# Performance work log

Measured on AMD Instinct MI355X. Metric: run time of the kernel, lower is better.

Reference implementation:

```python
import jax, jax.numpy as jnp
import numpy as np

K = 24  # number of clusters (all ids in [0,K) assumed present per image)
DELTA_VAR = 1.0
DELTA_DIST = 2.0
VAR_W = 1.0
DIST_W = 1.0
REG_W = 1.0


def setup_inputs() -> dict:
    key = jax.random.key(0)
    k1, k2 = jax.random.split(key)
    data = jax.random.normal(k1, (4, 16, 512, 1024), dtype=jnp.float32)
    labels = jax.random.randint(k2, (4, 512, 1024), 0, K, dtype=jnp.int32)
    return {"data": data, "labels": labels}


def reference(data, labels):
    B, D, H, Wd = data.shape
    N = H * Wd
    # [B, N, D] points, [B*N] global segment ids (batch-offset cluster ids)
    X = jnp.transpose(data.reshape(B, D, N), (0, 2, 1)).reshape(B * N, D)
    seg = (labels.reshape(B, N) + jnp.arange(B, dtype=labels.dtype)[:, None] * K).reshape(-1)

    # per-cluster sums and counts -> centers  [B*K, D]
    sums = jax.ops.segment_sum(X, seg, num_segments=B * K)
    counts = jax.ops.segment_sum(jnp.ones((B * N,), X.dtype), seg, num_segments=B * K)
    centers_flat = sums / counts[:, None]
    centers = centers_flat.reshape(B, K, D)
    counts_bk = counts.reshape(B, K)

    # variance term: per-point hinged distance to own cluster center
    c_per_point = centers_flat[seg]                      # [B*N, D]
    pt_dist = jnp.linalg.norm(X - c_per_point, axis=1)   # [B*N]
    hv = jnp.maximum(pt_dist - DELTA_VAR, 0.0) ** 2
    var_per_cluster = jax.ops.segment_sum(hv, seg, num_segments=B * K).reshape(B, K) / counts_bk
    var_sum = var_per_cluster.sum()

    # distance term: pairwise center distances (diagonal kept, as in original,
    # contributing a constant delta_dist**2 per cluster)
    diff = centers[:, :, None, :] - centers[:, None, :, :]     # [B, K, K, D]
    sq = jnp.sum(diff * diff, axis=-1)                         # [B, K, K]
    eye = jnp.eye(K, dtype=bool)[None]
    cdist = jnp.where(eye, 0.0, jnp.sqrt(jnp.where(eye, 1.0, sq)))
    hd = jnp.maximum(DELTA_DIST - cdist, 0.0) ** 2
    dist_sum = hd.sum() / (2.0 * K * (K - 1))

    # regularization: mean center norm per image, summed over batch
    reg_sum = jnp.linalg.norm(centers, axis=2).mean(axis=1).sum()

    loss = (VAR_W * var_sum + DIST_W * dist_sum + REG_W * reg_sum) / B
    return loss
```

## Files before the change

### kernel.cpp

```cpp
#include <hip/hip_runtime.h>
#include <math.h>

#define KC 24
constexpr int D = 16;
constexpr int B = 4;
constexpr int N = 512 * 1024;
constexpr float DELTA_VAR = 1.0f;
constexpr float DELTA_DIST = 2.0f;

constexpr int REP = 8;
constexpr int RS  = KC * 17;
constexpr int CS  = 33;
constexpr int PTS = 1024;
constexpr int BLOCKS = (B * N) / PTS;


__global__ __launch_bounds__(256) void k_sums(const float* __restrict__ data,
                                              const int* __restrict__ labels,
                                              float* __restrict__ g_sums,
                                              float* __restrict__ g_cnt) {
    __shared__ float s_sum[REP * RS];
    __shared__ float s_cnt[REP * CS];
    const int t = threadIdx.x;
    for (int i = t; i < REP * RS; i += 256) s_sum[i] = 0.f;
    for (int i = t; i < REP * CS; i += 256) s_cnt[i] = 0.f;
    __syncthreads();

    const int chunk = blockIdx.x * PTS;
    const int b     = chunk >> 19;
    const int n0    = (chunk & (N - 1)) + t * 4;

    const int4 lab = *(const int4*)(labels + chunk + t * 4);
    const int rbase = (t & 7) * RS;
    const int ax = rbase + lab.x * 17;
    const int ay = rbase + lab.y * 17;
    const int az = rbase + lab.z * 17;
    const int aw = rbase + lab.w * 17;

    const float* base = data + (size_t)(b * D) * N + n0;
    float4 cur = *(const float4*)(base);
#pragma unroll
    for (int d = 0; d < D; ++d) {
        float4 nxt;
        if (d < D - 1) nxt = *(const float4*)(base + (size_t)(d + 1) * N);
        atomicAdd(&s_sum[ax + d], cur.x);
        atomicAdd(&s_sum[ay + d], cur.y);
        atomicAdd(&s_sum[az + d], cur.z);
        atomicAdd(&s_sum[aw + d], cur.w);
        cur = nxt;
    }
    const int cbase = (t & 7) * CS;
    atomicAdd(&s_cnt[cbase + lab.x], 1.f);
    atomicAdd(&s_cnt[cbase + lab.y], 1.f);
    atomicAdd(&s_cnt[cbase + lab.z], 1.f);
    atomicAdd(&s_cnt[cbase + lab.w], 1.f);
    __syncthreads();

    const int rot = (blockIdx.x * 131) & 255;
    for (int i = t; i < KC * D; i += 256) {
        int j = (i + rot) % (KC * D);
        int c = j >> 4, d = j & 15;
        float s = 0.f;
#pragma unroll
        for (int r = 0; r < REP; ++r) s += s_sum[r * RS + c * 17 + d];
        atomicAdd(&g_sums[b * (KC * D) + j], s);
    }
    if (t < KC) {
        float s = 0.f;
#pragma unroll
        for (int r = 0; r < REP; ++r) s += s_cnt[r * CS + t];
        atomicAdd(&g_cnt[b * KC + t], s);
    }
}

__global__ __launch_bounds__(256) void k_var(const float* __restrict__ data,
                                             const int* __restrict__ labels,
                                             const float* __restrict__ g_sums,
                                             const float* __restrict__ g_cnt,
                                             float* __restrict__ g_varp) {
    __shared__ float s_c[KC * 17];
    __shared__ float s_ic[KC];
    __shared__ float s_part[4];
    const int t = threadIdx.x;
    const int chunk = blockIdx.x * PTS;
    const int b     = chunk >> 19;
    const int n0    = (chunk & (N - 1)) + t * 4;

    for (int i = t; i < KC * D; i += 256) {
        int c = i >> 4, d = i & 15;
        s_c[c * 17 + d] = g_sums[b * (KC * D) + i] / g_cnt[b * KC + c];
    }
    if (t < KC) s_ic[t] = 1.f / g_cnt[b * KC + t];
    __syncthreads();

    const int4 lab = *(const int4*)(labels + chunk + t * 4);
    const int ax = lab.x * 17, ay = lab.y * 17, az = lab.z * 17, aw = lab.w * 17;

    const float* base = data + (size_t)(b * D) * N + n0;
    float4 acc = {0.f, 0.f, 0.f, 0.f};
    float4 cur = *(const float4*)(base);
#pragma unroll
    for (int d = 0; d < D; ++d) {
        float4 nxt;
        if (d < D - 1) nxt = *(const float4*)(base + (size_t)(d + 1) * N);
        float df;
        df = cur.x - s_c[ax + d]; acc.x += df * df;
        df = cur.y - s_c[ay + d]; acc.y += df * df;
        df = cur.z - s_c[az + d]; acc.z += df * df;
        df = cur.w - s_c[aw + d]; acc.w += df * df;
        cur = nxt;
    }
    float h, hsum;
    h = fmaxf(sqrtf(acc.x) - DELTA_VAR, 0.f); hsum  = h * h * s_ic[lab.x];
    h = fmaxf(sqrtf(acc.y) - DELTA_VAR, 0.f); hsum += h * h * s_ic[lab.y];
    h = fmaxf(sqrtf(acc.z) - DELTA_VAR, 0.f); hsum += h * h * s_ic[lab.z];
    h = fmaxf(sqrtf(acc.w) - DELTA_VAR, 0.f); hsum += h * h * s_ic[lab.w];

    for (int o = 32; o > 0; o >>= 1) hsum += __shfl_down(hsum, o, 64);
    if ((t & 63) == 0) s_part[t >> 6] = hsum;
    __syncthreads();
    if (t == 0)
        atomicAdd(&g_varp[blockIdx.x & 63],
                  s_part[0] + s_part[1] + s_part[2] + s_part[3]);
}

__global__ __launch_bounds__(128) void k_final(const float* __restrict__ g_sums,
                                               const float* __restrict__ g_cnt,
                                               const float* __restrict__ g_varp,
                                               float* __restrict__ out) {
    __shared__ float s_c[B * KC * 17];
    __shared__ float s_red[2];
    const int t = threadIdx.x;

    float acc = 0.f;
    if (t < B * KC) {
        float cnt = g_cnt[t];
        float ns = 0.f;
        for (int d = 0; d < D; ++d) {
            float c = g_sums[t * D + d] / cnt;
            s_c[t * 17 + d] = c;
            ns += c * c;
        }
        acc = sqrtf(ns) / (float)KC;
    }
    if (t < 64) acc += g_varp[t];
    __syncthreads();

    float dacc = 0.f;
    for (int idx = t; idx < B * KC * KC; idx += 128) {
        int b = idx / (KC * KC);
        int r = idx % (KC * KC);
        int i = r / KC, j = r % KC;
        float hd;
        if (i == j) {
            hd = DELTA_DIST * DELTA_DIST;
        } else {
            const float* ci = &s_c[(b * KC + i) * 17];
            const float* cj = &s_c[(b * KC + j) * 17];
            float sq = 0.f;
            for (int d = 0; d < D; ++d) { float df = ci[d] - cj[d]; sq += df * df; }
            float hh = fmaxf(DELTA_DIST - sqrtf(sq), 0.f);
            hd = hh * hh;
        }
        dacc += hd;
    }
    float total = acc + dacc / (2.f * KC * (KC - 1));

    for (int o = 32; o > 0; o >>= 1) total += __shfl_down(total, o, 64);
    if ((t & 63) == 0) s_red[t >> 6] = total;
    __syncthreads();
    if (t == 0) out[0] = (s_red[0] + s_red[1]) / (float)B;
}

extern "C" void kernel_launch(void* const* d_in, const int* in_sizes, int n_in,
                              void* d_out, int out_size, void* d_ws, size_t ws_size,
                              hipStream_t stream) {
    const float* data  = (const float*)d_in[0];
    const int* labels  = (const int*)d_in[1];
    float* ws = (float*)d_ws;
    float* g_sums = ws;
    float* g_cnt  = ws + B * KC * D;
    float* g_varp = g_cnt + B * KC;

    hipMemsetAsync(d_ws, 0, (B * KC * D + B * KC + 64) * sizeof(float), stream);

    k_sums<<<BLOCKS, 256, 0, stream>>>(data, labels, g_sums, g_cnt);
    k_var <<<BLOCKS, 256, 0, stream>>>(data, labels, g_sums, g_cnt, g_varp);
    k_final<<<1, 128, 0, stream>>>(g_sums, g_cnt, g_varp, (float*)d_out);
}
```

Baseline: 356.2 us.

## Split cluster-sum kernel per channel chunk and double points per var-kernel thread

The sum kernel now assigns each block one (batch, channel, 16K-point chunk), so shared-memory histograms shrink to 24 bins per replica and each block issues many fewer global atomics. The trade-off is that labels are re-read once per channel, 16 times in total. The variance kernel now processes two float4 groups per thread over 2048 points per block, halving block count and centre-loading overhead. This adds register pressure and drops the explicit software prefetch.

```diff
diff --git a/kernel.cpp b/kernel.cpp
--- a/kernel.cpp
+++ b/kernel.cpp
@@ -9,67 +9,71 @@
 constexpr float DELTA_DIST = 2.0f;
 
 constexpr int REP = 8;
-constexpr int RS  = KC * 17;
 constexpr int CS  = 33;
-constexpr int PTS = 1024;
-constexpr int BLOCKS = (B * N) / PTS;
+constexpr int CHUNK = 16384;
+constexpr int NCH = N / CHUNK;
+constexpr int SBLOCKS = B * D * NCH;
+
+constexpr int VPTS = 2048;
+constexpr int VBLOCKS = (B * N) / VPTS;
 
 
 __global__ __launch_bounds__(256) void k_sums(const float* __restrict__ data,
                                               const int* __restrict__ labels,
                                               float* __restrict__ g_sums,
                                               float* __restrict__ g_cnt) {
-    __shared__ float s_sum[REP * RS];
+    __shared__ float s_sum[REP * CS];
     __shared__ float s_cnt[REP * CS];
-    const int t = threadIdx.x;
-    for (int i = t; i < REP * RS; i += 256) s_sum[i] = 0.f;
-    for (int i = t; i < REP * CS; i += 256) s_cnt[i] = 0.f;
-    __syncthreads();
-
-    const int chunk = blockIdx.x * PTS;
-    const int b     = chunk >> 19;
-    const int n0    = (chunk & (N - 1)) + t * 4;
-
-    const int4 lab = *(const int4*)(labels + chunk + t * 4);
-    const int rbase = (t & 7) * RS;
-    const int ax = rbase + lab.x * 17;
-    const int ay = rbase + lab.y * 17;
-    const int az = rbase + lab.z * 17;
-    const int aw = rbase + lab.w * 17;
-
-    const float* base = data + (size_t)(b * D) * N + n0;
-    float4 cur = *(const float4*)(base);
-#pragma unroll
-    for (int d = 0; d < D; ++d) {
-        float4 nxt;
-        if (d < D - 1) nxt = *(const float4*)(base + (size_t)(d + 1) * N);
-        atomicAdd(&s_sum[ax + d], cur.x);
-        atomicAdd(&s_sum[ay + d], cur.y);
-        atomicAdd(&s_sum[az + d], cur.z);
-        atomicAdd(&s_sum[aw + d], cur.w);
-        cur = nxt;
-    }
-    const int cbase = (t & 7) * CS;
-    atomicAdd(&s_cnt[cbase + lab.x], 1.f);
-    atomicAdd(&s_cnt[cbase + lab.y], 1.f);
-    atomicAdd(&s_cnt[cbase + lab.z], 1.f);
-    atomicAdd(&s_cnt[cbase + lab.w], 1.f);
-    __syncthreads();
-
-    const int rot = (blockIdx.x * 131) & 255;
-    for (int i = t; i < KC * D; i += 256) {
-        int j = (i + rot) % (KC * D);
-        int c = j >> 4, d = j & 15;
-        float s = 0.f;
-#pragma unroll
-        for (int r = 0; r < REP; ++r) s += s_sum[r * RS + c * 17 + d];
-        atomicAdd(&g_sums[b * (KC * D) + j], s);
-    }
+    const int t   = threadIdx.x;
+    const int idx = blockIdx.x;
+    const int d   = idx & 15;
+    const int c   = (idx >> 4) & (NCH - 1);
+    const int b   = idx >> 9;
+
+    for (int i = t; i < REP * CS; i += 256) { s_sum[i] = 0.f; s_cnt[i] = 0.f; }
+    __syncthreads();
+
+    const float* dp = data  + ((size_t)b * D + d) * N + (size_t)c * CHUNK;
+    const int*   lp = labels + (size_t)b * N          + (size_t)c * CHUNK;
+    const int rb = (t & 7) * CS;
+
+    if (d == 0) {
+        for (int i = t * 4; i < CHUNK; i += 1024) {
+            float4 v = *(const float4*)(dp + i);
+            int4   l = *(const int4*)(lp + i);
+            atomicAdd(&s_sum[rb + l.x], v.x);
+            atomicAdd(&s_sum[rb + l.y], v.y);
+            atomicAdd(&s_sum[rb + l.z], v.z);
+            atomicAdd(&s_sum[rb + l.w], v.w);
+            atomicAdd(&s_cnt[rb + l.x], 1.f);
+            atomicAdd(&s_cnt[rb + l.y], 1.f);
+            atomicAdd(&s_cnt[rb + l.z], 1.f);
+            atomicAdd(&s_cnt[rb + l.w], 1.f);
+        }
+    } else {
+        for (int i = t * 4; i < CHUNK; i += 1024) {
+            float4 v = *(const float4*)(dp + i);
+            int4   l = *(const int4*)(lp + i);
+            atomicAdd(&s_sum[rb + l.x], v.x);
+            atomicAdd(&s_sum[rb + l.y], v.y);
+            atomicAdd(&s_sum[rb + l.z], v.z);
+            atomicAdd(&s_sum[rb + l.w], v.w);
+        }
+    }
+    __syncthreads();
+
     if (t < KC) {
         float s = 0.f;
 #pragma unroll
-        for (int r = 0; r < REP; ++r) s += s_cnt[r * CS + t];
-        atomicAdd(&g_cnt[b * KC + t], s);
+        for (int r = 0; r < REP; ++r) s += s_sum[r * CS + t];
+        atomicAdd(&g_sums[(b * KC + t) * D + d], s);
+    }
+    if (d == 0 && t >= 64 && t < 64 + KC) {
+        const int k = t - 64;
+        float s = 0.f;
+#pragma unroll
+        for (int r = 0; r < REP; ++r) s += s_cnt[r * CS + k];
+        atomicAdd(&g_cnt[b * KC + k], s);
     }
 }
 
@@ -82,39 +86,48 @@
     __shared__ float s_ic[KC];
     __shared__ float s_part[4];
     const int t = threadIdx.x;
-    const int chunk = blockIdx.x * PTS;
+    const int chunk = blockIdx.x * VPTS;
     const int b     = chunk >> 19;
-    const int n0    = (chunk & (N - 1)) + t * 4;
+    const int n0    = chunk & (N - 1);
 
     for (int i = t; i < KC * D; i += 256) {
-        int c = i >> 4, d = i & 15;
-        s_c[c * 17 + d] = g_sums[b * (KC * D) + i] / g_cnt[b * KC + c];
+        int k = i >> 4, d = i & 15;
+        s_c[k * 17 + d] = g_sums[i + b * (KC * D)] / g_cnt[b * KC + k];
     }
     if (t < KC) s_ic[t] = 1.f / g_cnt[b * KC + t];
     __syncthreads();
 
-    const int4 lab = *(const int4*)(labels + chunk + t * 4);
-    const int ax = lab.x * 17, ay = lab.y * 17, az = lab.z * 17, aw = lab.w * 17;
-
-    const float* base = data + (size_t)(b * D) * N + n0;
-    float4 acc = {0.f, 0.f, 0.f, 0.f};
-    float4 cur = *(const float4*)(base);
+    const int4 l0 = *(const int4*)(labels + chunk + t * 4);
+    const int4 l1 = *(const int4*)(labels + chunk + 1024 + t * 4);
+    const int a0x = l0.x * 17, a0y = l0.y * 17, a0z = l0.z * 17, a0w = l0.w * 17;
+    const int a1x = l1.x * 17, a1y = l1.y * 17, a1z = l1.z * 17, a1w = l1.w * 17;
+
+    const float* base = data + (size_t)(b * D) * N + n0 + t * 4;
+    float4 q0 = {0.f, 0.f, 0.f, 0.f};
+    float4 q1 = {0.f, 0.f, 0.f, 0.f};
 #pragma unroll
     for (int d = 0; d < D; ++d) {
-        float4 nxt;
-        if (d < D - 1) nxt = *(const float4*)(base + (size_t)(d + 1) * N);
+        float4 v0 = *(const float4*)(base + (size_t)d * N);
+        float4 v1 = *(const float4*)(base + (size_t)d * N + 1024);
         float df;
-        df = cur.x - s_c[ax + d]; acc.x += df * df;
-        df = cur.y - s_c[ay + d]; acc.y += df * df;
-        df = cur.z - s_c[az + d]; acc.z += df * df;
-        df = cur.w - s_c[aw + d]; acc.w += df * df;
-        cur = nxt;
+        df = v0.x - s_c[a0x + d]; q0.x += df * df;
+        df = v0.y - s_c[a0y + d]; q0.y += df * df;
+        df = v0.z - s_c[a0z + d]; q0.z += df * df;
+        df = v0.w - s_c[a0w + d]; q0.w += df * df;
+        df = v1.x - s_c[a1x + d]; q1.x += df * df;
+        df = v1.y - s_c[a1y + d]; q1.y += df * df;
+        df = v1.z - s_c[a1z + d]; q1.z += df * df;
+        df = v1.w - s_c[a1w + d]; q1.w += df * df;
     }
     float h, hsum;
-    h = fmaxf(sqrtf(acc.x) - DELTA_VAR, 0.f); hsum  = h * h * s_ic[lab.x];
-    h = fmaxf(sqrtf(acc.y) - DELTA_VAR, 0.f); hsum += h * h * s_ic[lab.y];
-    h = fmaxf(sqrtf(acc.z) - DELTA_VAR, 0.f); hsum += h * h * s_ic[lab.z];
-    h = fmaxf(sqrtf(acc.w) - DELTA_VAR, 0.f); hsum += h * h * s_ic[lab.w];
+    h = fmaxf(sqrtf(q0.x) - DELTA_VAR, 0.f); hsum  = h * h * s_ic[l0.x];
+    h = fmaxf(sqrtf(q0.y) - DELTA_VAR, 0.f); hsum += h * h * s_ic[l0.y];
+    h = fmaxf(sqrtf(q0.z) - DELTA_VAR, 0.f); hsum += h * h * s_ic[l0.z];
+    h = fmaxf(sqrtf(q0.w) - DELTA_VAR, 0.f); hsum += h * h * s_ic[l0.w];
+    h = fmaxf(sqrtf(q1.x) - DELTA_VAR, 0.f); hsum += h * h * s_ic[l1.x];
+    h = fmaxf(sqrtf(q1.y) - DELTA_VAR, 0.f); hsum += h * h * s_ic[l1.y];
+    h = fmaxf(sqrtf(q1.z) - DELTA_VAR, 0.f); hsum += h * h * s_ic[l1.z];
+    h = fmaxf(sqrtf(q1.w) - DELTA_VAR, 0.f); hsum += h * h * s_ic[l1.w];
 
     for (int o = 32; o > 0; o >>= 1) hsum += __shfl_down(hsum, o, 64);
     if ((t & 63) == 0) s_part[t >> 6] = hsum;
@@ -184,7 +197,7 @@
 
     hipMemsetAsync(d_ws, 0, (B * KC * D + B * KC + 64) * sizeof(float), stream);
 
-    k_sums<<<BLOCKS, 256, 0, stream>>>(data, labels, g_sums, g_cnt);
-    k_var <<<BLOCKS, 256, 0, stream>>>(data, labels, g_sums, g_cnt, g_varp);
+    k_sums<<<SBLOCKS, 256, 0, stream>>>(data, labels, g_sums, g_cnt);
+    k_var <<<VBLOCKS, 256, 0, stream>>>(data, labels, g_sums, g_cnt, g_varp);
     k_final<<<1, 128, 0, stream>>>(g_sums, g_cnt, g_varp, (float*)d_out);
 }
```

New measurement: 504.6 us. 41.7% more time.

## Fuse sums and variance passes into one cooperative kernel with bf16 register cache

Applied to the files above, without the earlier changes.

Merges the cluster-sum and variance kernels into one cooperative launch separated by a global atomic barrier. Each thread handles 8 points and keeps their features packed as bf16 in registers, so the input is read from memory only once. The variance distance is then computed from the bf16 copies. This trades precision in the variance term and occupancy (large 1024-thread blocks, many live registers) for halving global traffic and dropping a launch.

```diff
diff --git a/kernel.cpp b/kernel.cpp
--- a/kernel.cpp
+++ b/kernel.cpp
@@ -11,117 +11,148 @@
 constexpr int REP = 8;
 constexpr int RS  = KC * 17;
 constexpr int CS  = 33;
-constexpr int PTS = 1024;
-constexpr int BLOCKS = (B * N) / PTS;
-
-
-__global__ __launch_bounds__(256) void k_sums(const float* __restrict__ data,
-                                              const int* __restrict__ labels,
-                                              float* __restrict__ g_sums,
-                                              float* __restrict__ g_cnt) {
+constexpr int TPB = 1024;
+constexpr int GRID = 256;
+constexpr int PPT = 8;
+
+
+__device__ inline unsigned pk_bf16(float a, float b) {
+    unsigned ua = __float_as_uint(a), ub = __float_as_uint(b);
+    ua += 0x7fffu + ((ua >> 16) & 1u);
+    ub += 0x7fffu + ((ub >> 16) & 1u);
+    return (ua >> 16) | (ub & 0xffff0000u);
+}
+__device__ inline float lo_bf16(unsigned u) { return __uint_as_float(u << 16); }
+__device__ inline float hi_bf16(unsigned u) { return __uint_as_float(u & 0xffff0000u); }
+
+__global__ __launch_bounds__(TPB) void k_fused(const float* __restrict__ data,
+                                               const int* __restrict__ labels,
+                                               float* __restrict__ g_sums,
+                                               float* __restrict__ g_cnt,
+                                               float* __restrict__ g_varp,
+                                               int* __restrict__ g_bar) {
     __shared__ float s_sum[REP * RS];
     __shared__ float s_cnt[REP * CS];
+    __shared__ float s_c[KC * 20];
+    __shared__ float s_ic[KC];
+    __shared__ float s_part[TPB / 64];
     const int t = threadIdx.x;
-    for (int i = t; i < REP * RS; i += 256) s_sum[i] = 0.f;
-    for (int i = t; i < REP * CS; i += 256) s_cnt[i] = 0.f;
-    __syncthreads();
-
-    const int chunk = blockIdx.x * PTS;
-    const int b     = chunk >> 19;
-    const int n0    = (chunk & (N - 1)) + t * 4;
-
-    const int4 lab = *(const int4*)(labels + chunk + t * 4);
-    const int rbase = (t & 7) * RS;
-    const int ax = rbase + lab.x * 17;
-    const int ay = rbase + lab.y * 17;
-    const int az = rbase + lab.z * 17;
-    const int aw = rbase + lab.w * 17;
-
-    const float* base = data + (size_t)(b * D) * N + n0;
-    float4 cur = *(const float4*)(base);
+    for (int i = t; i < REP * RS; i += TPB) s_sum[i] = 0.f;
+    for (int i = t; i < REP * CS; i += TPB) s_cnt[i] = 0.f;
+    __syncthreads();
+
+    const int p0 = (blockIdx.x * TPB + t) * PPT;
+    const int b  = p0 >> 19;
+    const int n0 = p0 & (N - 1);
+
+    const int4 la = *(const int4*)(labels + p0);
+    const int4 lb = *(const int4*)(labels + p0 + 4);
+
+    const int rb = (t & 7) * RS;
+    const int ax0 = rb + la.x * 17, ax1 = rb + la.y * 17, ax2 = rb + la.z * 17, ax3 = rb + la.w * 17;
+    const int ax4 = rb + lb.x * 17, ax5 = rb + lb.y * 17, ax6 = rb + lb.z * 17, ax7 = rb + lb.w * 17;
+
+    unsigned u[D][4];
+    const float* dp0 = data + (size_t)(b * D) * N + n0;
 #pragma unroll
     for (int d = 0; d < D; ++d) {
-        float4 nxt;
-        if (d < D - 1) nxt = *(const float4*)(base + (size_t)(d + 1) * N);
-        atomicAdd(&s_sum[ax + d], cur.x);
-        atomicAdd(&s_sum[ay + d], cur.y);
-        atomicAdd(&s_sum[az + d], cur.z);
-        atomicAdd(&s_sum[aw + d], cur.w);
-        cur = nxt;
-    }
-    const int cbase = (t & 7) * CS;
-    atomicAdd(&s_cnt[cbase + lab.x], 1.f);
-    atomicAdd(&s_cnt[cbase + lab.y], 1.f);
-    atomicAdd(&s_cnt[cbase + lab.z], 1.f);
-    atomicAdd(&s_cnt[cbase + lab.w], 1.f);
-    __syncthreads();
-
-    const int rot = (blockIdx.x * 131) & 255;
-    for (int i = t; i < KC * D; i += 256) {
-        int j = (i + rot) % (KC * D);
-        int c = j >> 4, d = j & 15;
+        const float* dp = dp0 + (size_t)d * N;
+        float4 v0 = *(const float4*)(dp);
+        float4 v1 = *(const float4*)(dp + 4);
+        atomicAdd(&s_sum[ax0 + d], v0.x);
+        atomicAdd(&s_sum[ax1 + d], v0.y);
+        atomicAdd(&s_sum[ax2 + d], v0.z);
+        atomicAdd(&s_sum[ax3 + d], v0.w);
+        atomicAdd(&s_sum[ax4 + d], v1.x);
+        atomicAdd(&s_sum[ax5 + d], v1.y);
+        atomicAdd(&s_sum[ax6 + d], v1.z);
+        atomicAdd(&s_sum[ax7 + d], v1.w);
+        u[d][0] = pk_bf16(v0.x, v0.y);
+        u[d][1] = pk_bf16(v0.z, v0.w);
+        u[d][2] = pk_bf16(v1.x, v1.y);
+        u[d][3] = pk_bf16(v1.z, v1.w);
+    }
+    {
+        const int cb = (t & 7) * CS;
+        atomicAdd(&s_cnt[cb + la.x], 1.f);
+        atomicAdd(&s_cnt[cb + la.y], 1.f);
+        atomicAdd(&s_cnt[cb + la.z], 1.f);
+        atomicAdd(&s_cnt[cb + la.w], 1.f);
+        atomicAdd(&s_cnt[cb + lb.x], 1.f);
+        atomicAdd(&s_cnt[cb + lb.y], 1.f);
+        atomicAdd(&s_cnt[cb + lb.z], 1.f);
+        atomicAdd(&s_cnt[cb + lb.w], 1.f);
+    }
+    __syncthreads();
+
+    if (t < KC * D) {
         float s = 0.f;
 #pragma unroll
-        for (int r = 0; r < REP; ++r) s += s_sum[r * RS + c * 17 + d];
-        atomicAdd(&g_sums[b * (KC * D) + j], s);
-    }
-    if (t < KC) {
+        for (int r = 0; r < REP; ++r) s += s_sum[r * RS + (t >> 4) * 17 + (t & 15)];
+        atomicAdd(&g_sums[b * (KC * D) + t], s);
+    } else if (t < KC * D + KC) {
+        const int k = t - KC * D;
         float s = 0.f;
 #pragma unroll
-        for (int r = 0; r < REP; ++r) s += s_cnt[r * CS + t];
-        atomicAdd(&g_cnt[b * KC + t], s);
-    }
-}
-
-__global__ __launch_bounds__(256) void k_var(const float* __restrict__ data,
-                                             const int* __restrict__ labels,
-                                             const float* __restrict__ g_sums,
-                                             const float* __restrict__ g_cnt,
-                                             float* __restrict__ g_varp) {
-    __shared__ float s_c[KC * 17];
-    __shared__ float s_ic[KC];
-    __shared__ float s_part[4];
-    const int t = threadIdx.x;
-    const int chunk = blockIdx.x * PTS;
-    const int b     = chunk >> 19;
-    const int n0    = (chunk & (N - 1)) + t * 4;
-
-    for (int i = t; i < KC * D; i += 256) {
-        int c = i >> 4, d = i & 15;
-        s_c[c * 17 + d] = g_sums[b * (KC * D) + i] / g_cnt[b * KC + c];
-    }
-    if (t < KC) s_ic[t] = 1.f / g_cnt[b * KC + t];
-    __syncthreads();
-
-    const int4 lab = *(const int4*)(labels + chunk + t * 4);
-    const int ax = lab.x * 17, ay = lab.y * 17, az = lab.z * 17, aw = lab.w * 17;
-
-    const float* base = data + (size_t)(b * D) * N + n0;
-    float4 acc = {0.f, 0.f, 0.f, 0.f};
-    float4 cur = *(const float4*)(base);
-#pragma unroll
-    for (int d = 0; d < D; ++d) {
-        float4 nxt;
-        if (d < D - 1) nxt = *(const float4*)(base + (size_t)(d + 1) * N);
-        float df;
-        df = cur.x - s_c[ax + d]; acc.x += df * df;
-        df = cur.y - s_c[ay + d]; acc.y += df * df;
-        df = cur.z - s_c[az + d]; acc.z += df * df;
-        df = cur.w - s_c[aw + d]; acc.w += df * df;
-        cur = nxt;
-    }
-    float h, hsum;
-    h = fmaxf(sqrtf(acc.x) - DELTA_VAR, 0.f); hsum  = h * h * s_ic[lab.x];
-    h = fmaxf(sqrtf(acc.y) - DELTA_VAR, 0.f); hsum += h * h * s_ic[lab.y];
-    h = fmaxf(sqrtf(acc.z) - DELTA_VAR, 0.f); hsum += h * h * s_ic[lab.z];
-    h = fmaxf(sqrtf(acc.w) - DELTA_VAR, 0.f); hsum += h * h * s_ic[lab.w];
+        for (int r = 0; r < REP; ++r) s += s_cnt[r * CS + k];
+        atomicAdd(&g_cnt[b * KC + k], s);
+    }
+
+    __threadfence();
+    __syncthreads();
+    if (t == 0) {
+        __hip_atomic_fetch_add(g_bar, 1, __ATOMIC_ACQ_REL, __HIP_MEMORY_SCOPE_AGENT);
+        while (__hip_atomic_load(g_bar, __ATOMIC_ACQUIRE, __HIP_MEMORY_SCOPE_AGENT) < GRID)
+            __builtin_amdgcn_s_sleep(2);
+    }
+    __syncthreads();
+
+    if (t < KC)
+        s_ic[t] = 1.0f / __hip_atomic_load(&g_cnt[b * KC + t],
+                                           __ATOMIC_RELAXED, __HIP_MEMORY_SCOPE_AGENT);
+    __syncthreads();
+    if (t < KC * D) {
+        float s = __hip_atomic_load(&g_sums[b * (KC * D) + t],
+                                    __ATOMIC_RELAXED, __HIP_MEMORY_SCOPE_AGENT);
+        s_c[(t >> 4) * 20 + (t & 15)] = s * s_ic[t >> 4];
+    }
+    __syncthreads();
+
+    float hsum = 0.f;
+#define PT(LAB, HALF, J) do {                                             \
+        const float* cp = &s_c[(LAB) * 20];                               \
+        float ce[D];                                                      \
+        _Pragma("unroll")                                                 \
+        for (int d4 = 0; d4 < 4; ++d4) {                                  \
+            float4 cv = *(const float4*)(cp + 4 * d4);                    \
+            ce[4 * d4] = cv.x; ce[4 * d4 + 1] = cv.y;                     \
+            ce[4 * d4 + 2] = cv.z; ce[4 * d4 + 3] = cv.w;                 \
+        }                                                                 \
+        float q = 0.f;                                                    \
+        _Pragma("unroll")                                                 \
+        for (int d = 0; d < D; ++d) {                                     \
+            float x = (HALF) ? hi_bf16(u[d][J]) : lo_bf16(u[d][J]);       \
+            float df = x - ce[d]; q += df * df;                           \
+        }                                                                 \
+        float h = fmaxf(sqrtf(q) - DELTA_VAR, 0.f);                       \
+        hsum += h * h * s_ic[LAB];                                        \
+    } while (0)
+
+    PT(la.x, 0, 0); PT(la.y, 1, 0);
+    PT(la.z, 0, 1); PT(la.w, 1, 1);
+    PT(lb.x, 0, 2); PT(lb.y, 1, 2);
+    PT(lb.z, 0, 3); PT(lb.w, 1, 3);
+#undef PT
 
     for (int o = 32; o > 0; o >>= 1) hsum += __shfl_down(hsum, o, 64);
     if ((t & 63) == 0) s_part[t >> 6] = hsum;
     __syncthreads();
-    if (t == 0)
-        atomicAdd(&g_varp[blockIdx.x & 63],
-                  s_part[0] + s_part[1] + s_part[2] + s_part[3]);
+    if (t == 0) {
+        float s = 0.f;
+#pragma unroll
+        for (int w = 0; w < TPB / 64; ++w) s += s_part[w];
+        atomicAdd(&g_varp[blockIdx.x & 63], s);
+    }
 }
 
 __global__ __launch_bounds__(128) void k_final(const float* __restrict__ g_sums,
@@ -181,10 +212,13 @@
     float* g_sums = ws;
     float* g_cnt  = ws + B * KC * D;
     float* g_varp = g_cnt + B * KC;
-
-    hipMemsetAsync(d_ws, 0, (B * KC * D + B * KC + 64) * sizeof(float), stream);
-
-    k_sums<<<BLOCKS, 256, 0, stream>>>(data, labels, g_sums, g_cnt);
-    k_var <<<BLOCKS, 256, 0, stream>>>(data, labels, g_sums, g_cnt, g_varp);
+    int*   g_bar  = (int*)(g_varp + 64);
+
+    hipMemsetAsync(d_ws, 0, (B * KC * D + B * KC + 64 + 4) * sizeof(float), stream);
+
+    void* args[] = {(void*)&data, (void*)&labels, (void*)&g_sums,
+                    (void*)&g_cnt, (void*)&g_varp, (void*)&g_bar};
+    hipLaunchCooperativeKernel((const void*)k_fused, dim3(GRID), dim3(TPB),
+                               args, 0, stream);
     k_final<<<1, 128, 0, stream>>>(g_sums, g_cnt, g_varp, (float*)d_out);
 }
```

New measurement: 444.8 us. 1.25x slower.
